# Kernel tuning notes

Hardware: AMD Instinct MI355X
Metric: run time of the kernel (lower is better)

## Reference

```python
import jax, jax.numpy as jnp
import numpy as np

N_NODES = 50000
N_EDGES = 800000
N_GRAPHS = 500
IN_CH = 128
HID = 128
OUT_CH = 10
N_LAYERS = 3


def setup_inputs() -> dict:
    key = jax.random.key(0)
    ks = jax.random.split(key, 12)
    s_in = 1.0 / np.sqrt(IN_CH)
    s_h = 1.0 / np.sqrt(HID)
    inp = {
        "x": jax.random.normal(ks[0], (N_NODES, IN_CH), jnp.float32),
        "conv_w1": jax.random.normal(ks[1], (N_LAYERS, HID, HID), jnp.float32) * s_in,
        "conv_b1": jax.random.normal(ks[2], (N_LAYERS, HID), jnp.float32) * s_in,
        "conv_w2": jax.random.normal(ks[3], (N_LAYERS, HID, HID), jnp.float32) * s_h,
        "conv_b2": jax.random.normal(ks[4], (N_LAYERS, HID), jnp.float32) * s_h,
        "mlp_w1": jax.random.normal(ks[5], (HID, HID), jnp.float32) * s_h,
        "mlp_b1": jax.random.normal(ks[6], (HID,), jnp.float32) * s_h,
        "mlp_w2": jax.random.normal(ks[7], (HID, OUT_CH), jnp.float32) * s_h,
        "mlp_b2": jax.random.normal(ks[8], (OUT_CH,), jnp.float32) * s_h,
        "edge_index": jax.random.randint(ks[9], (2, N_EDGES), 0, N_NODES, jnp.int64),
        "batch": jnp.sort(jax.random.randint(ks[10], (N_NODES,), 0, N_GRAPHS, jnp.int64)),
    }
    return inp


def reference(x, conv_w1, conv_b1, conv_w2, conv_b2,
              mlp_w1, mlp_b1, mlp_w2, mlp_b2, edge_index, batch):
    src, dst = edge_index[0], edge_index[1]
    n = x.shape[0]
    for l in range(conv_w1.shape[0]):
        # GINConv, eps=0: h_i = mlp(x_i + sum_{j in N(i)} x_j)
        agg = jax.ops.segment_sum(x[src], dst, num_segments=n)  # [N, d]
        h = x + agg
        h = jnp.maximum(h @ conv_w1[l] + conv_b1[l], 0.0) @ conv_w2[l] + conv_b2[l]
        x = jnp.maximum(h, 0.0)  # outer F.relu(conv(...))
    # global_add_pool over graph ids
    g = jax.ops.segment_sum(x, batch, num_segments=N_GRAPHS)  # [G, HID]
    # final MLP (dropout is identity in eval)
    h = jnp.maximum(g @ mlp_w1 + mlp_b1, 0.0)
    return h @ mlp_w2 + mlp_b2
```

## Files before the change

kernel.cpp:

```cpp
#include <hip/hip_runtime.h>

#define NODES   50000
#define EDGES   800000
#define GRAPHS  500
#define HID     128
#define OUTC    10
#define NLAYERS 3
#define ELLCAP  64

typedef __bf16 bf16x8 __attribute__((ext_vector_type(8)));
typedef float  f32x4  __attribute__((ext_vector_type(4)));

__device__ __forceinline__ unsigned short f2bf(float f){
    unsigned u = __float_as_uint(f);
    u = (u + 0x7fffu + ((u >> 16) & 1u)) >> 16;
    return (unsigned short)u;
}
__device__ __forceinline__ float bf2f(unsigned short h){
    return __uint_as_float(((unsigned)h) << 16);
}

#define FILLB  ((EDGES + 255) / 256)
#define PREPB  ((6 * HID * HID + 255) / 256)
#define CONVB  ((NODES * 64 + 255) / 256)

__global__ __launch_bounds__(256) void setup_kernel(
    const int* __restrict__ src, const int* __restrict__ dst,
    int* __restrict__ deg, unsigned short* __restrict__ ell,
    const float* __restrict__ w1, const float* __restrict__ w2,
    unsigned short* __restrict__ wt,
    const float* __restrict__ x, unsigned* __restrict__ xb)
{
    const int b = blockIdx.x;
    if (b < FILLB) {
        int e = b * 256 + threadIdx.x;
        if (e < EDGES) {
            int d = dst[e];
            int pos = atomicAdd(&deg[d], 1);
            if (pos < ELLCAP)
                ell[(size_t)pos * NODES + d] = (unsigned short)src[e];
        }
    } else if (b < FILLB + PREPB) {
        int idx = (b - FILLB) * 256 + threadIdx.x;
        if (idx < 6 * HID * HID) {
            int m = idx >> 14;
            int n = (idx >> 7) & 127;
            int k = idx & 127;
            const float* w = (m < 3) ? (w1 + (size_t)m * HID * HID)
                                     : (w2 + (size_t)(m - 3) * HID * HID);
            wt[idx] = f2bf(w[(size_t)k * HID + n]);
        }
    } else {
        int i = (b - FILLB - PREPB) * 256 + threadIdx.x;
        if (i < NODES * 64) {
            float2 v = reinterpret_cast<const float2*>(x)[i];
            xb[i] = ((unsigned)f2bf(v.y) << 16) | f2bf(v.x);
        }
    }
}

__global__ __launch_bounds__(512) void layer_kernel(
    const unsigned short* __restrict__ X,
    const int* __restrict__ deg, const unsigned short* __restrict__ ell,
    const unsigned short* __restrict__ Wt1, const float* __restrict__ bias1,
    const unsigned short* __restrict__ Wt2, const float* __restrict__ bias2,
    unsigned short* __restrict__ C)
{
    __shared__ unsigned short As[32][136];
    __shared__ unsigned short idx_s[ELLCAP][32];
    __shared__ int deg_s[32];
    const int tid  = threadIdx.x;
    const int w    = tid >> 6;
    const int lane = tid & 63;
    const int q    = lane >> 4;
    const int lr   = lane & 15;
    const int row0 = blockIdx.x * 32;

    const uint4* xr = reinterpret_cast<const uint4*>(X);

    if (tid < 32) {
        int n = row0 + tid;
        if (n >= NODES) n = NODES - 1;
        deg_s[tid] = min(deg[n], ELLCAP);
    }
    __syncthreads();

    int maxd = 0;
    #pragma unroll
    for (int i = 0; i < 32; ++i) maxd = max(maxd, deg_s[i]);

    {
        const int sl0 = tid >> 5;
        const int nn  = tid & 31;
        int gn = row0 + nn;
        if (gn >= NODES) gn = NODES - 1;
        for (int s = sl0; s < maxd; s += 16)
            idx_s[s][nn] = ell[(size_t)s * NODES + gn];
    }
    __syncthreads();

    for (int i = 0; i < 4; ++i) {
        const int row = w * 4 + i;
        int n = row0 + row;
        if (n >= NODES) n = NODES - 1;

        float acc[8];
        #pragma unroll
        for (int k = 0; k < 8; ++k) acc[k] = 0.f;

        const int dg = deg_s[row];
        for (int e0 = 0; e0 < dg; e0 += 16) {
            uint4 v[4];
            unsigned m[4];
            #pragma unroll
            for (int j = 0; j < 4; ++j) {
                int e = e0 + 4 * j + q;
                bool ok = e < dg;
                m[j] = ok ? 0xffffffffu : 0u;
                int ec = ok ? e : (dg - 1);
                int s = idx_s[ec][row];
                v[j] = xr[(size_t)s * 16 + lr];
            }
            #pragma unroll
            for (int j = 0; j < 4; ++j) {
                const unsigned uu[4] = {v[j].x, v[j].y, v[j].z, v[j].w};
                #pragma unroll
                for (int k2 = 0; k2 < 4; ++k2) {
                    unsigned uv = uu[k2] & m[j];
                    acc[2 * k2]     += __uint_as_float(uv << 16);
                    acc[2 * k2 + 1] += __uint_as_float(uv & 0xffff0000u);
                }
            }
        }

        #pragma unroll
        for (int k = 0; k < 8; ++k) {
            acc[k] += __shfl_xor(acc[k], 16, 64);
            acc[k] += __shfl_xor(acc[k], 32, 64);
        }

        if (q == 0) {
            uint4 self = xr[(size_t)n * 16 + lr];
            const unsigned su[4] = {self.x, self.y, self.z, self.w};
            uint4 o;
            unsigned* ou = &o.x;
            #pragma unroll
            for (int j = 0; j < 4; ++j) {
                float c0 = acc[2 * j]     + __uint_as_float(su[j] << 16);
                float c1 = acc[2 * j + 1] + __uint_as_float(su[j] & 0xffff0000u);
                ou[j] = ((unsigned)f2bf(c1) << 16) | f2bf(c0);
            }
            *reinterpret_cast<uint4*>(&As[row][lr * 8]) = o;
        }
    }
    __syncthreads();

    const int rg = w >> 2;
    const int cq = w & 3;
    const int ar = rg * 16 + lr;

    bf16x8 af[4];
    f32x4 acc[2];

    #pragma unroll
    for (int s = 0; s < 4; ++s)
        af[s] = *reinterpret_cast<const bf16x8*>(&As[ar][s * 32 + q * 8]);
    __syncthreads();

    #pragma unroll
    for (int nt = 0; nt < 2; ++nt) acc[nt] = (f32x4){0.f, 0.f, 0.f, 0.f};
    {
        #pragma unroll
        for (int nt = 0; nt < 2; ++nt) {
            const unsigned short* wn = Wt1 + (size_t)(cq * 32 + nt * 16 + lr) * HID + q * 8;
            #pragma unroll
            for (int s = 0; s < 4; ++s) {
                bf16x8 b = *reinterpret_cast<const bf16x8*>(wn + s * 32);
                acc[nt] = __builtin_amdgcn_mfma_f32_16x16x32_bf16(b, af[s], acc[nt], 0, 0, 0);
            }
        }
    }

    {
        const float4* b4p = reinterpret_cast<const float4*>(bias1);
        #pragma unroll
        for (int nt = 0; nt < 2; ++nt) {
            int col = cq * 32 + nt * 16 + q * 4;
            float4 b4 = b4p[col >> 2];
            ushort4 o;
            o.x = f2bf(fmaxf(acc[nt][0] + b4.x, 0.f));
            o.y = f2bf(fmaxf(acc[nt][1] + b4.y, 0.f));
            o.z = f2bf(fmaxf(acc[nt][2] + b4.z, 0.f));
            o.w = f2bf(fmaxf(acc[nt][3] + b4.w, 0.f));
            *reinterpret_cast<ushort4*>(&As[ar][col]) = o;
        }
    }
    __syncthreads();

    #pragma unroll
    for (int s = 0; s < 4; ++s)
        af[s] = *reinterpret_cast<const bf16x8*>(&As[ar][s * 32 + q * 8]);
    #pragma unroll
    for (int nt = 0; nt < 2; ++nt) acc[nt] = (f32x4){0.f, 0.f, 0.f, 0.f};
    {
        #pragma unroll
        for (int nt = 0; nt < 2; ++nt) {
            const unsigned short* wn = Wt2 + (size_t)(cq * 32 + nt * 16 + lr) * HID + q * 8;
            #pragma unroll
            for (int s = 0; s < 4; ++s) {
                bf16x8 b = *reinterpret_cast<const bf16x8*>(wn + s * 32);
                acc[nt] = __builtin_amdgcn_mfma_f32_16x16x32_bf16(b, af[s], acc[nt], 0, 0, 0);
            }
        }
    }

    const int row = row0 + ar;
    if (row < NODES) {
        const float4* b4p = reinterpret_cast<const float4*>(bias2);
        #pragma unroll
        for (int nt = 0; nt < 2; ++nt) {
            int col = cq * 32 + nt * 16 + q * 4;
            float4 b4 = b4p[col >> 2];
            ushort4 o;
            o.x = f2bf(fmaxf(acc[nt][0] + b4.x, 0.f));
            o.y = f2bf(fmaxf(acc[nt][1] + b4.y, 0.f));
            o.z = f2bf(fmaxf(acc[nt][2] + b4.z, 0.f));
            o.w = f2bf(fmaxf(acc[nt][3] + b4.w, 0.f));
            *reinterpret_cast<ushort4*>(C + (size_t)row * HID + col) = o;
        }
    }
}

__device__ __forceinline__ int lbound(const int* __restrict__ a, int v)
{
    int lo = 0, hi = NODES;
    while (lo < hi) {
        int m = (lo + hi) >> 1;
        if (a[m] < v) lo = m + 1; else hi = m;
    }
    return lo;
}

__global__ __launch_bounds__(256) void pool_sorted_kernel(
    const unsigned short* __restrict__ x,
    const int* __restrict__ batch,
    float* __restrict__ g)
{
    const int gid = blockIdx.x;
    const int beg = lbound(batch, gid);
    const int end = lbound(batch, gid + 1);

    const int c    = threadIdx.x & 127;
    const int half = threadIdx.x >> 7;

    float acc = 0.f;
    for (int r = beg + half; r < end; r += 2)
        acc += bf2f(x[(size_t)r * HID + c]);

    __shared__ float lds[256];
    lds[threadIdx.x] = acc;
    __syncthreads();
    if (threadIdx.x < 128)
        g[(size_t)gid * HID + threadIdx.x] = lds[threadIdx.x] + lds[threadIdx.x + 128];
}

__global__ __launch_bounds__(256) void gemm128_f32_kernel(
    const float* __restrict__ A,
    const float* __restrict__ W,
    const float* __restrict__ bias,
    float* __restrict__ C,
    int M)
{
    __shared__ float As[32][HID];
    const int tid  = threadIdx.x;
    const int row0 = blockIdx.x * 32;

    {
        const int r = tid >> 3;
        const int c = (tid & 7) * 16;
        const int gr = row0 + r;
        float4* ps = reinterpret_cast<float4*>(&As[r][c]);
        if (gr < M) {
            const float4* pa = reinterpret_cast<const float4*>(A + (size_t)gr * HID + c);
            #pragma unroll
            for (int j = 0; j < 4; ++j) ps[j] = pa[j];
        } else {
            #pragma unroll
            for (int j = 0; j < 4; ++j) ps[j] = make_float4(0.f, 0.f, 0.f, 0.f);
        }
    }
    __syncthreads();

    const int tx = tid & 31;
    const int ty = tid >> 5;

    float4 acc[4];
    #pragma unroll
    for (int i = 0; i < 4; ++i) acc[i] = make_float4(0.f, 0.f, 0.f, 0.f);

    #pragma unroll 4
    for (int k = 0; k < HID; ++k) {
        const float4 w = *reinterpret_cast<const float4*>(W + (size_t)k * HID + tx * 4);
        #pragma unroll
        for (int i = 0; i < 4; ++i) {
            const float a = As[ty + 8 * i][k];
            acc[i].x += a * w.x;
            acc[i].y += a * w.y;
            acc[i].z += a * w.z;
            acc[i].w += a * w.w;
        }
    }

    const float4 b4 = *reinterpret_cast<const float4*>(bias + tx * 4);
    #pragma unroll
    for (int i = 0; i < 4; ++i) {
        const int row = row0 + ty + 8 * i;
        if (row < M) {
            float4 o = make_float4(fmaxf(acc[i].x + b4.x, 0.f),
                                   fmaxf(acc[i].y + b4.y, 0.f),
                                   fmaxf(acc[i].z + b4.z, 0.f),
                                   fmaxf(acc[i].w + b4.w, 0.f));
            *reinterpret_cast<float4*>(C + (size_t)row * HID + tx * 4) = o;
        }
    }
}

__global__ __launch_bounds__(256) void final_kernel(
    const float* __restrict__ gh,
    const float* __restrict__ w2,
    const float* __restrict__ b2,
    float* __restrict__ out)
{
    int idx = blockIdx.x * 256 + threadIdx.x;
    int r = idx >> 4;
    int c = idx & 15;
    if (r >= GRAPHS || c >= OUTC) return;
    float acc = b2[c];
    for (int k = 0; k < HID; ++k)
        acc += gh[(size_t)r * HID + k] * w2[(size_t)k * OUTC + c];
    out[(size_t)r * OUTC + c] = acc;
}

extern "C" void kernel_launch(void* const* d_in, const int* in_sizes, int n_in,
                              void* d_out, int out_size, void* d_ws, size_t ws_size,
                              hipStream_t stream)
{
    const float* x    = (const float*)d_in[0];
    const float* w1   = (const float*)d_in[1];
    const float* b1   = (const float*)d_in[2];
    const float* w2   = (const float*)d_in[3];
    const float* b2   = (const float*)d_in[4];
    const float* mw1  = (const float*)d_in[5];
    const float* mb1  = (const float*)d_in[6];
    const float* mw2  = (const float*)d_in[7];
    const float* mb2  = (const float*)d_in[8];
    const int*   ei   = (const int*)d_in[9];
    const int*   batch= (const int*)d_in[10];
    float* out = (float*)d_out;

    char* p = (char*)d_ws;
    unsigned short* buf0 = (unsigned short*)p;  p += (size_t)NODES * HID * 2;
    unsigned short* buf1 = (unsigned short*)p;  p += (size_t)NODES * HID * 2;
    unsigned short* ell  = (unsigned short*)p;  p += (size_t)NODES * ELLCAP * 2;
    unsigned short* wt   = (unsigned short*)p;  p += (size_t)6 * HID * HID * 2;
    float* g      = (float*)p;                  p += (size_t)GRAPHS * HID * 4;
    float* gh     = (float*)p;                  p += (size_t)GRAPHS * HID * 4;
    int*   deg    = (int*)p;                    p += (size_t)NODES * 4;

    const int* src = ei;
    const int* dst = ei + EDGES;

    const int layerBlocks = (NODES + 31) / 32;
    const int setupBlocks = FILLB + PREPB + CONVB;

    hipMemsetAsync(deg, 0, (size_t)NODES * sizeof(int), stream);
    setup_kernel<<<setupBlocks, 256, 0, stream>>>(
        src, dst, deg, ell, w1, w2, wt, x, (unsigned*)buf0);

    unsigned short* bin  = buf0;
    unsigned short* bout = buf1;
    for (int l = 0; l < NLAYERS; ++l) {
        layer_kernel<<<layerBlocks, 512, 0, stream>>>(
            bin, deg, ell,
            wt + (size_t)l * HID * HID,       b1 + (size_t)l * HID,
            wt + (size_t)(l + 3) * HID * HID, b2 + (size_t)l * HID,
            bout);
        unsigned short* t = bin; bin = bout; bout = t;
    }

    pool_sorted_kernel<<<GRAPHS, 256, 0, stream>>>(bin, batch, g);
    gemm128_f32_kernel<<<(GRAPHS + 31) / 32, 256, 0, stream>>>(g, mw1, mb1, gh, GRAPHS);
    final_kernel<<<(GRAPHS * 16 + 255) / 256, 256, 0, stream>>>(gh, mw2, mb2, out);
}
```

Baseline: 256.8 us.

## Split features into column halves and separate gather from dual GEMM

Node features are now stored as two 64-column halves (half-major layout), so each neighbor-gather pass only touches a 6.4 MB slab. That slab is more likely to stay cache-resident during the random gathers. The fused layer kernel is split into a gather kernel, launched over both halves, that writes the aggregated input to a buffer, and a separate dual-GEMM kernel that reads it back. This adds an extra kernel launch per layer and a round trip of the aggregated activations through memory, in exchange for better gather locality.

After: 316.9 us. +23.4%, slower.

```diff
diff --git a/kernel.cpp b/kernel.cpp
--- a/kernel.cpp
+++ b/kernel.cpp
@@ -7,6 +7,7 @@
 #define OUTC    10
 #define NLAYERS 3
 #define ELLCAP  64
+#define NTILES  1563
 
 typedef __bf16 bf16x8 __attribute__((ext_vector_type(8)));
 typedef float  f32x4  __attribute__((ext_vector_type(4)));
@@ -54,33 +55,36 @@
         int i = (b - FILLB - PREPB) * 256 + threadIdx.x;
         if (i < NODES * 64) {
             float2 v = reinterpret_cast<const float2*>(x)[i];
-            xb[i] = ((unsigned)f2bf(v.y) << 16) | f2bf(v.x);
-        }
-    }
-}
-
-__global__ __launch_bounds__(512) void layer_kernel(
+            int node = i >> 6;
+            int pr   = i & 63;
+            int hc   = pr >> 5;
+            xb[((size_t)hc * NODES + node) * 32 + (pr & 31)] =
+                ((unsigned)f2bf(v.y) << 16) | f2bf(v.x);
+        }
+    }
+}
+
+__global__ __launch_bounds__(512) void gather_pass_kernel(
     const unsigned short* __restrict__ X,
     const int* __restrict__ deg, const unsigned short* __restrict__ ell,
-    const unsigned short* __restrict__ Wt1, const float* __restrict__ bias1,
-    const unsigned short* __restrict__ Wt2, const float* __restrict__ bias2,
-    unsigned short* __restrict__ C)
-{
-    __shared__ unsigned short As[32][136];
+    unsigned short* __restrict__ hin)
+{
     __shared__ unsigned short idx_s[ELLCAP][32];
     __shared__ int deg_s[32];
     const int tid  = threadIdx.x;
+    const int bid  = blockIdx.x;
+    const int pass = bid / NTILES;
+    const int row0 = (bid - pass * NTILES) * 32;
     const int w    = tid >> 6;
     const int lane = tid & 63;
-    const int q    = lane >> 4;
-    const int lr   = lane & 15;
-    const int row0 = blockIdx.x * 32;
-
-    const uint4* xr = reinterpret_cast<const uint4*>(X);
+    const int q8   = lane >> 3;
+    const int l8   = lane & 7;
+
+    const uint4* xr = reinterpret_cast<const uint4*>(X) + (size_t)pass * NODES * 8;
+    uint4*       hr = reinterpret_cast<uint4*>(hin)     + (size_t)pass * NODES * 8;
 
     if (tid < 32) {
-        int n = row0 + tid;
-        if (n >= NODES) n = NODES - 1;
+        int n = row0 + tid; if (n >= NODES) n = NODES - 1;
         deg_s[tid] = min(deg[n], ELLCAP);
     }
     __syncthreads();
@@ -90,10 +94,8 @@
     for (int i = 0; i < 32; ++i) maxd = max(maxd, deg_s[i]);
 
     {
-        const int sl0 = tid >> 5;
-        const int nn  = tid & 31;
-        int gn = row0 + nn;
-        if (gn >= NODES) gn = NODES - 1;
+        const int sl0 = tid >> 5, nn = tid & 31;
+        int gn = row0 + nn; if (gn >= NODES) gn = NODES - 1;
         for (int s = sl0; s < maxd; s += 16)
             idx_s[s][nn] = ell[(size_t)s * NODES + gn];
     }
@@ -101,8 +103,7 @@
 
     for (int i = 0; i < 4; ++i) {
         const int row = w * 4 + i;
-        int n = row0 + row;
-        if (n >= NODES) n = NODES - 1;
+        int n = row0 + row; if (n >= NODES) n = NODES - 1;
 
         float acc[8];
         #pragma unroll
@@ -110,19 +111,18 @@
 
         const int dg = deg_s[row];
         for (int e0 = 0; e0 < dg; e0 += 16) {
-            uint4 v[4];
-            unsigned m[4];
-            #pragma unroll
-            for (int j = 0; j < 4; ++j) {
-                int e = e0 + 4 * j + q;
+            uint4 v[2]; unsigned m[2];
+            #pragma unroll
+            for (int j = 0; j < 2; ++j) {
+                int e = e0 + j * 8 + q8;
                 bool ok = e < dg;
                 m[j] = ok ? 0xffffffffu : 0u;
-                int ec = ok ? e : (dg - 1);
+                int ec = ok ? e : 0;
                 int s = idx_s[ec][row];
-                v[j] = xr[(size_t)s * 16 + lr];
+                v[j] = xr[(size_t)s * 8 + l8];
             }
             #pragma unroll
-            for (int j = 0; j < 4; ++j) {
+            for (int j = 0; j < 2; ++j) {
                 const unsigned uu[4] = {v[j].x, v[j].y, v[j].z, v[j].w};
                 #pragma unroll
                 for (int k2 = 0; k2 < 4; ++k2) {
@@ -135,23 +135,47 @@
 
         #pragma unroll
         for (int k = 0; k < 8; ++k) {
+            acc[k] += __shfl_xor(acc[k], 8, 64);
             acc[k] += __shfl_xor(acc[k], 16, 64);
             acc[k] += __shfl_xor(acc[k], 32, 64);
         }
 
-        if (q == 0) {
-            uint4 self = xr[(size_t)n * 16 + lr];
+        if (q8 == 0) {
+            uint4 self = xr[(size_t)n * 8 + l8];
             const unsigned su[4] = {self.x, self.y, self.z, self.w};
-            uint4 o;
-            unsigned* ou = &o.x;
-            #pragma unroll
-            for (int j = 0; j < 4; ++j) {
-                float c0 = acc[2 * j]     + __uint_as_float(su[j] << 16);
-                float c1 = acc[2 * j + 1] + __uint_as_float(su[j] & 0xffff0000u);
-                ou[j] = ((unsigned)f2bf(c1) << 16) | f2bf(c0);
+            uint4 o; unsigned* ou = &o.x;
+            #pragma unroll
+            for (int jj = 0; jj < 4; ++jj) {
+                float c0 = acc[2 * jj]     + __uint_as_float(su[jj] << 16);
+                float c1 = acc[2 * jj + 1] + __uint_as_float(su[jj] & 0xffff0000u);
+                ou[jj] = ((unsigned)f2bf(c1) << 16) | f2bf(c0);
             }
-            *reinterpret_cast<uint4*>(&As[row][lr * 8]) = o;
-        }
+            hr[(size_t)n * 8 + l8] = o;
+        }
+    }
+}
+
+__global__ __launch_bounds__(512) void gemm_dual_kernel(
+    const unsigned short* __restrict__ A,
+    const unsigned short* __restrict__ Wt1, const float* __restrict__ bias1,
+    const unsigned short* __restrict__ Wt2, const float* __restrict__ bias2,
+    unsigned short* __restrict__ C)
+{
+    __shared__ unsigned short As[32][136];
+    const int tid  = threadIdx.x;
+    const int w    = tid >> 6;
+    const int lane = tid & 63;
+    const int q    = lane >> 4;
+    const int lr   = lane & 15;
+    const int row0 = blockIdx.x * 32;
+
+    {
+        int r  = tid >> 4;
+        int cw = tid & 15;
+        int gr = row0 + r; if (gr >= NODES) gr = NODES - 1;
+        int half = cw >> 3;
+        uint4 v = reinterpret_cast<const uint4*>(A)[((size_t)half * NODES + gr) * 8 + (cw & 7)];
+        *reinterpret_cast<uint4*>(&As[r][cw * 8]) = v;
     }
     __syncthreads();
 
@@ -226,7 +250,9 @@
             o.y = f2bf(fmaxf(acc[nt][1] + b4.y, 0.f));
             o.z = f2bf(fmaxf(acc[nt][2] + b4.z, 0.f));
             o.w = f2bf(fmaxf(acc[nt][3] + b4.w, 0.f));
-            *reinterpret_cast<ushort4*>(C + (size_t)row * HID + col) = o;
+            int half = col >> 6;
+            *reinterpret_cast<ushort4*>(
+                C + ((size_t)half * NODES + row) * 64 + (col & 63)) = o;
         }
     }
 }
@@ -250,12 +276,14 @@
     const int beg = lbound(batch, gid);
     const int end = lbound(batch, gid + 1);
 
-    const int c    = threadIdx.x & 127;
-    const int half = threadIdx.x >> 7;
+    const int c  = threadIdx.x & 127;
+    const int hp = threadIdx.x >> 7;
+    const int ch = c >> 6;
+    const int co = c & 63;
 
     float acc = 0.f;
-    for (int r = beg + half; r < end; r += 2)
-        acc += bf2f(x[(size_t)r * HID + c]);
+    for (int r = beg + hp; r < end; r += 2)
+        acc += bf2f(x[((size_t)ch * NODES + r) * 64 + co]);
 
     __shared__ float lds[256];
     lds[threadIdx.x] = acc;
@@ -370,7 +398,6 @@
     const int* src = ei;
     const int* dst = ei + EDGES;
 
-    const int layerBlocks = (NODES + 31) / 32;
     const int setupBlocks = FILLB + PREPB + CONVB;
 
     hipMemsetAsync(deg, 0, (size_t)NODES * sizeof(int), stream);
@@ -380,12 +407,12 @@
     unsigned short* bin  = buf0;
     unsigned short* bout = buf1;
     for (int l = 0; l < NLAYERS; ++l) {
-        layer_kernel<<<layerBlocks, 512, 0, stream>>>(
-            bin, deg, ell,
+        gather_pass_kernel<<<2 * NTILES, 512, 0, stream>>>(bin, deg, ell, bout);
+        gemm_dual_kernel<<<NTILES, 512, 0, stream>>>(
+            bout,
             wt + (size_t)l * HID * HID,       b1 + (size_t)l * HID,
             wt + (size_t)(l + 3) * HID * HID, b2 + (size_t)l * HID,
-            bout);
-        unsigned short* t = bin; bin = bout; bout = t;
+            bin);
     }
 
     pool_sorted_kernel<<<GRAPHS, 256, 0, stream>>>(bin, batch, g);
```

## Bucket edges by destination range before ELL fill; fuse pool with final MLP

Applied to the files above, without the earlier changes.

Edge insertion now runs in two passes. First, edges are binned into 8 destination-range buckets using per-block local counters, packed as (local dst, src). A second kernel then does the per-node atomic ELL fill within each bucket, so the scattered atomics and writes land in a smaller address range and get better cache locality. The pooling, hidden MLP and output layer are fused into one per-graph kernel, which removes two launches and the intermediate global buffers. In exchange the fill adds an extra kernel launch and a round trip through a packed edge buffer, and the padded-gather index now points at slot 0 rather than the last edge.

Measured after the change: 275.8 us. 1.07x slower.

```diff
diff --git a/kernel.cpp b/kernel.cpp
--- a/kernel.cpp
+++ b/kernel.cpp
@@ -20,25 +20,43 @@
     return __uint_as_float(((unsigned)h) << 16);
 }
 
+#define FGRPS  8
+#define GSZ    (NODES / FGRPS)
+#define GCAP   131072
 #define FILLB  ((EDGES + 255) / 256)
 #define PREPB  ((6 * HID * HID + 255) / 256)
 #define CONVB  ((NODES * 64 + 255) / 256)
+#define FPB2   98
 
 __global__ __launch_bounds__(256) void setup_kernel(
     const int* __restrict__ src, const int* __restrict__ dst,
-    int* __restrict__ deg, unsigned short* __restrict__ ell,
+    unsigned* __restrict__ ep, int* __restrict__ gcnt,
     const float* __restrict__ w1, const float* __restrict__ w2,
     unsigned short* __restrict__ wt,
     const float* __restrict__ x, unsigned* __restrict__ xb)
 {
     const int b = blockIdx.x;
     if (b < FILLB) {
-        int e = b * 256 + threadIdx.x;
-        if (e < EDGES) {
-            int d = dst[e];
-            int pos = atomicAdd(&deg[d], 1);
-            if (pos < ELLCAP)
-                ell[(size_t)pos * NODES + d] = (unsigned short)src[e];
+        __shared__ int lcnt[FGRPS], lbase[FGRPS];
+        const int tid = threadIdx.x;
+        int e = b * 256 + tid;
+        if (tid < FGRPS) lcnt[tid] = 0;
+        __syncthreads();
+        int d = 0, s = 0, grp = 0, lpos = 0;
+        bool ok = e < EDGES;
+        if (ok) {
+            d = dst[e]; s = src[e];
+            grp = d / GSZ;
+            lpos = atomicAdd(&lcnt[grp], 1);
+        }
+        __syncthreads();
+        if (tid < FGRPS) lbase[tid] = atomicAdd(&gcnt[tid], lcnt[tid]);
+        __syncthreads();
+        if (ok) {
+            int pos = lbase[grp] + lpos;
+            if (pos < GCAP)
+                ep[(size_t)grp * GCAP + pos] =
+                    ((unsigned)(d - grp * GSZ) << 16) | (unsigned)s;
         }
     } else if (b < FILLB + PREPB) {
         int idx = (b - FILLB) * 256 + threadIdx.x;
@@ -59,6 +77,24 @@
     }
 }
 
+__global__ __launch_bounds__(256) void fill2_kernel(
+    const unsigned* __restrict__ ep, const int* __restrict__ gcnt,
+    int* __restrict__ deg, unsigned short* __restrict__ ell)
+{
+    const int grp = blockIdx.x & 7;
+    const int bi  = blockIdx.x >> 3;
+    const int n0  = grp * GSZ;
+    const int cnt = min(gcnt[grp], GCAP);
+    const unsigned* p = ep + (size_t)grp * GCAP;
+    for (int e = bi * 256 + threadIdx.x; e < cnt; e += FPB2 * 256) {
+        unsigned r = p[e];
+        int d = n0 + (int)(r >> 16);
+        int s = (int)(r & 0xffffu);
+        int pos = atomicAdd(&deg[d], 1);
+        if (pos < ELLCAP) ell[(size_t)pos * NODES + d] = (unsigned short)s;
+    }
+}
+
 __global__ __launch_bounds__(512) void layer_kernel(
     const unsigned short* __restrict__ X,
     const int* __restrict__ deg, const unsigned short* __restrict__ ell,
@@ -117,7 +153,7 @@
                 int e = e0 + 4 * j + q;
                 bool ok = e < dg;
                 m[j] = ok ? 0xffffffffu : 0u;
-                int ec = ok ? e : (dg - 1);
+                int ec = ok ? e : 0;
                 int s = idx_s[ec][row];
                 v[j] = xr[(size_t)s * 16 + lr];
             }
@@ -241,10 +277,12 @@
     return lo;
 }
 
-__global__ __launch_bounds__(256) void pool_sorted_kernel(
+__global__ __launch_bounds__(256) void pool_mlp_kernel(
     const unsigned short* __restrict__ x,
     const int* __restrict__ batch,
-    float* __restrict__ g)
+    const float* __restrict__ mw1, const float* __restrict__ mb1,
+    const float* __restrict__ mw2, const float* __restrict__ mb2,
+    float* __restrict__ out)
 {
     const int gid = blockIdx.x;
     const int beg = lbound(batch, gid);
@@ -258,87 +296,30 @@
         acc += bf2f(x[(size_t)r * HID + c]);
 
     __shared__ float lds[256];
+    __shared__ float gl[128];
+    __shared__ float gh[128];
     lds[threadIdx.x] = acc;
     __syncthreads();
     if (threadIdx.x < 128)
-        g[(size_t)gid * HID + threadIdx.x] = lds[threadIdx.x] + lds[threadIdx.x + 128];
-}
-
-__global__ __launch_bounds__(256) void gemm128_f32_kernel(
-    const float* __restrict__ A,
-    const float* __restrict__ W,
-    const float* __restrict__ bias,
-    float* __restrict__ C,
-    int M)
-{
-    __shared__ float As[32][HID];
-    const int tid  = threadIdx.x;
-    const int row0 = blockIdx.x * 32;
-
-    {
-        const int r = tid >> 3;
-        const int c = (tid & 7) * 16;
-        const int gr = row0 + r;
-        float4* ps = reinterpret_cast<float4*>(&As[r][c]);
-        if (gr < M) {
-            const float4* pa = reinterpret_cast<const float4*>(A + (size_t)gr * HID + c);
-            #pragma unroll
-            for (int j = 0; j < 4; ++j) ps[j] = pa[j];
-        } else {
-            #pragma unroll
-            for (int j = 0; j < 4; ++j) ps[j] = make_float4(0.f, 0.f, 0.f, 0.f);
-        }
-    }
-    __syncthreads();
-
-    const int tx = tid & 31;
-    const int ty = tid >> 5;
-
-    float4 acc[4];
-    #pragma unroll
-    for (int i = 0; i < 4; ++i) acc[i] = make_float4(0.f, 0.f, 0.f, 0.f);
-
-    #pragma unroll 4
-    for (int k = 0; k < HID; ++k) {
-        const float4 w = *reinterpret_cast<const float4*>(W + (size_t)k * HID + tx * 4);
-        #pragma unroll
-        for (int i = 0; i < 4; ++i) {
-            const float a = As[ty + 8 * i][k];
-            acc[i].x += a * w.x;
-            acc[i].y += a * w.y;
-            acc[i].z += a * w.z;
-            acc[i].w += a * w.w;
-        }
-    }
-
-    const float4 b4 = *reinterpret_cast<const float4*>(bias + tx * 4);
-    #pragma unroll
-    for (int i = 0; i < 4; ++i) {
-        const int row = row0 + ty + 8 * i;
-        if (row < M) {
-            float4 o = make_float4(fmaxf(acc[i].x + b4.x, 0.f),
-                                   fmaxf(acc[i].y + b4.y, 0.f),
-                                   fmaxf(acc[i].z + b4.z, 0.f),
-                                   fmaxf(acc[i].w + b4.w, 0.f));
-            *reinterpret_cast<float4*>(C + (size_t)row * HID + tx * 4) = o;
-        }
-    }
-}
-
-__global__ __launch_bounds__(256) void final_kernel(
-    const float* __restrict__ gh,
-    const float* __restrict__ w2,
-    const float* __restrict__ b2,
-    float* __restrict__ out)
-{
-    int idx = blockIdx.x * 256 + threadIdx.x;
-    int r = idx >> 4;
-    int c = idx & 15;
-    if (r >= GRAPHS || c >= OUTC) return;
-    float acc = b2[c];
-    for (int k = 0; k < HID; ++k)
-        acc += gh[(size_t)r * HID + k] * w2[(size_t)k * OUTC + c];
-    out[(size_t)r * OUTC + c] = acc;
+        gl[threadIdx.x] = lds[threadIdx.x] + lds[threadIdx.x + 128];
+    __syncthreads();
+
+    if (threadIdx.x < 128) {
+        float a = mb1[threadIdx.x];
+        #pragma unroll 8
+        for (int k = 0; k < 128; ++k)
+            a += gl[k] * mw1[(size_t)k * HID + threadIdx.x];
+        gh[threadIdx.x] = fmaxf(a, 0.f);
+    }
+    __syncthreads();
+
+    if (threadIdx.x < OUTC) {
+        float a = mb2[threadIdx.x];
+        #pragma unroll 8
+        for (int k = 0; k < 128; ++k)
+            a += gh[k] * mw2[(size_t)k * OUTC + threadIdx.x];
+        out[(size_t)gid * OUTC + threadIdx.x] = a;
+    }
 }
 
 extern "C" void kernel_launch(void* const* d_in, const int* in_sizes, int n_in,
@@ -363,9 +344,9 @@
     unsigned short* buf1 = (unsigned short*)p;  p += (size_t)NODES * HID * 2;
     unsigned short* ell  = (unsigned short*)p;  p += (size_t)NODES * ELLCAP * 2;
     unsigned short* wt   = (unsigned short*)p;  p += (size_t)6 * HID * HID * 2;
-    float* g      = (float*)p;                  p += (size_t)GRAPHS * HID * 4;
-    float* gh     = (float*)p;                  p += (size_t)GRAPHS * HID * 4;
+    unsigned* ep  = (unsigned*)p;               p += (size_t)FGRPS * GCAP * 4;
     int*   deg    = (int*)p;                    p += (size_t)NODES * 4;
+    int*   gcnt   = (int*)p;                    p += FGRPS * 4;
 
     const int* src = ei;
     const int* dst = ei + EDGES;
@@ -373,9 +354,10 @@
     const int layerBlocks = (NODES + 31) / 32;
     const int setupBlocks = FILLB + PREPB + CONVB;
 
-    hipMemsetAsync(deg, 0, (size_t)NODES * sizeof(int), stream);
+    hipMemsetAsync(deg, 0, ((size_t)NODES + FGRPS) * sizeof(int), stream);
     setup_kernel<<<setupBlocks, 256, 0, stream>>>(
-        src, dst, deg, ell, w1, w2, wt, x, (unsigned*)buf0);
+        src, dst, ep, gcnt, w1, w2, wt, x, (unsigned*)buf0);
+    fill2_kernel<<<FGRPS * FPB2, 256, 0, stream>>>(ep, gcnt, deg, ell);
 
     unsigned short* bin  = buf0;
     unsigned short* bout = buf1;
@@ -388,7 +370,5 @@
         unsigned short* t = bin; bin = bout; bout = t;
     }
 
-    pool_sorted_kernel<<<GRAPHS, 256, 0, stream>>>(bin, batch, g);
-    gemm128_f32_kernel<<<(GRAPHS + 31) / 32, 256, 0, stream>>>(g, mw1, mb1, gh, GRAPHS);
-    final_kernel<<<(GRAPHS * 16 + 255) / 256, 256, 0, stream>>>(gh, mw2, mb2, out);
-}
+    pool_mlp_kernel<<<GRAPHS, 256, 0, stream>>>(bin, batch, mw1, mb1, mw2, mb2, out);
+}
```
